# Kernel optimization log

Hardware: AMD Instinct MI355X
Metric: run time of the kernel (lower is better)

The kernel has to match this reference:

```python
import jax, jax.numpy as jnp
import numpy as np

MARGIN = 0.3
CLST_SCALE = 0.8
SEP_SCALE = 0.08
DIV_SCALE = 0.01
CONTRASTIVE_SCALE = 0.1


def setup_inputs() -> dict:
    key = jax.random.key(0)
    k1, k2, k3 = jax.random.split(key, 3)
    B, C, P, D = 16384, 100, 10, 256
    similarities = jax.random.uniform(k1, (B, C, P), jnp.float32, -1.0, 1.0)
    labels = jax.random.randint(k2, (B,), 0, C)
    prototypes = jax.random.normal(k3, (C * P, D), jnp.float32)
    starts = jnp.arange(C) * P
    proto_indices = jnp.stack([starts, starts + P], axis=1)  # [C,2] contiguous segments
    valid_mask = jnp.ones((C * P,), dtype=bool)
    return dict(similarities=similarities, labels=labels, prototypes=prototypes,
                proto_indices=proto_indices, valid_mask=valid_mask, max_prototypes=P)


def _balanced_proto_loss(similarities, prototypes, labels, proto_indices, valid_mask):
    B, C, P = similarities.shape
    T = prototypes.shape[0]
    distances = 1.0 - similarities  # [B,C,P]
    starts = proto_indices[:, 0]
    ends = proto_indices[:, 1]
    counts = ends - starts  # protos per class [C]
    INF = jnp.asarray(jnp.inf, distances.dtype)

    # mask invalid prototype slots per class, min over prototype slots
    pvalid = jnp.arange(P)[None, :] < counts[:, None]          # [C,P]
    dmask = jnp.where(pvalid[None, :, :], distances, INF)      # [B,C,P]
    min_all = jnp.min(dmask, axis=-1)                          # [B,C]

    # ---- cluster loss: min distance to own-class prototypes, class-balanced ----
    own_min = jnp.take_along_axis(min_all, labels[:, None], axis=1)[:, 0]  # [B]
    cls_n = jax.ops.segment_sum(jnp.ones_like(own_min), labels, num_segments=C)  # [C]
    cls_sum = jax.ops.segment_sum(own_min, labels, num_segments=C)
    has = cls_n > 0
    nvalid = jnp.maximum(jnp.sum(has), 1)
    mean_c = cls_sum / jnp.maximum(cls_n, 1.0)
    w = 1.0 / jnp.sqrt(cls_n + 1e-6)
    cluster_loss = jnp.sum(jnp.where(has, w * mean_c, 0.0)) / nvalid * CLST_SCALE

    # ---- separation loss: nearest prototype among all OTHER classes ----
    own_cls = jax.nn.one_hot(labels, C, dtype=bool)            # [B,C]
    other_min = jnp.min(jnp.where(own_cls, INF, min_all), axis=-1)  # [B]
    sep_term = jax.nn.relu(MARGIN - other_min)
    sep_cls_sum = jax.ops.segment_sum(sep_term, labels, num_segments=C)
    sep_loss = jnp.sum(jnp.where(has, sep_cls_sum / jnp.maximum(cls_n, 1.0), 0.0)) / nvalid * SEP_SCALE

    # ---- diversity loss: within-class prototype pairwise similarity (off-diagonal) ----
    norm = jnp.sqrt(jnp.sum(prototypes * prototypes, axis=-1, keepdims=True))
    pn = prototypes / jnp.maximum(norm, 1e-12)                 # F.normalize, eps=1e-12
    sim = pn @ pn.T                                            # [T,T]
    proto_class = jnp.searchsorted(starts, jnp.arange(T), side='right') - 1  # [T]
    same = proto_class[:, None] == proto_class[None, :]
    offdiag = ~jnp.eye(T, dtype=bool)
    pair = same & offdiag
    rel = jax.nn.relu(sim - 0.5)
    row_sum = jnp.sum(jnp.where(pair, rel, 0.0), axis=1)       # [T]
    cls_pair_sum = jax.ops.segment_sum(row_sum, proto_class, num_segments=C)
    npairs = (counts * (counts - 1)).astype(sim.dtype)
    div_valid = counts > 1
    ndv = jnp.maximum(jnp.sum(div_valid), 1)
    div_loss = jnp.sum(jnp.where(div_valid, cls_pair_sum / jnp.maximum(npairs, 1.0), 0.0)) / ndv * DIV_SCALE

    # ---- contrastive loss: mean off-diagonal sim over valid prototypes ----
    vpair = (valid_mask[:, None] & valid_mask[None, :]) & offdiag
    n_vpair = jnp.maximum(jnp.sum(vpair), 1).astype(sim.dtype)
    contrastive_loss = jnp.sum(jnp.where(vpair, sim, 0.0)) / n_vpair * CONTRASTIVE_SCALE

    total = cluster_loss + sep_loss + div_loss + contrastive_loss
    return jnp.stack([cluster_loss, sep_loss, div_loss, contrastive_loss, total])


def reference(similarities, labels, prototypes, proto_indices, valid_mask, max_prototypes):
    return _balanced_proto_loss(similarities, prototypes, labels, proto_indices, valid_mask)
```

## Files before the change

### kernel.cpp

```cpp
#include <hip/hip_runtime.h>
#include <hip/hip_bf16.h>
#include <math.h>

#define MARGIN_C 0.3f
#define CLST_SCALE 0.8f
#define SEP_SCALE 0.08f
#define DIV_SCALE 0.01f
#define CONTRASTIVE_SCALE 0.1f

#define INFF __builtin_huge_valf()
#define NVEC 16

__global__ __launch_bounds__(256) void norm_init_kernel(
    const float* __restrict__ protos, float* __restrict__ inv_norm,
    float* __restrict__ svec, double* __restrict__ diag,
    unsigned* __restrict__ done, int T, int D) {
    int t = threadIdx.x;
    if (blockIdx.x == 0) {
        for (int i = t; i < D; i += 256) svec[i] = 0.0f;
        if (t == 0) { *diag = 0.0; *done = 0u; }
    }
    int w = (blockIdx.x * 256 + t) >> 6;
    int lane = t & 63;
    if (w >= T) return;
    const float* row = protos + (size_t)w * D;
    float ss = 0.0f;
    if ((D & 3) == 0) {
        for (int k = lane * 4; k < D; k += 256) {
            float4 v = *reinterpret_cast<const float4*>(row + k);
            ss += v.x * v.x + v.y * v.y + v.z * v.z + v.w * v.w;
        }
    } else {
        for (int k = lane; k < D; k += 64) { float v = row[k]; ss += v * v; }
    }
#pragma unroll
    for (int off = 32; off > 0; off >>= 1) ss += __shfl_xor(ss, off);
    if (lane == 0) inv_norm[w] = 1.0f / fmaxf(sqrtf(ss), 1e-12f);
}

__global__ __launch_bounds__(256) void sample_kernel(
    const float* __restrict__ sims, const int* __restrict__ labels,
    const int* __restrict__ pidx,
    float* __restrict__ own_arr, float* __restrict__ sep_arr,
    int B, int C, int P) {
    int gid = blockIdx.x * 256 + threadIdx.x;
    int w = gid >> 6;
    int lane = threadIdx.x & 63;
    if (w >= B) return;
    int label = labels[w];
    const float* base = sims + (size_t)w * C * P;
    float own = INFF, other = INFF;
    for (int cc = 0; cc < C; cc += 64) {
        int c = cc + lane;
        if (c < C) {
            int cnt = pidx[2 * c + 1] - pidx[2 * c];
            const float* cb = base + (size_t)c * P;
            float m = INFF;
            if ((P & 1) == 0) {
                for (int p = 0; p < P; p += 2) {
                    float2 v = *reinterpret_cast<const float2*>(cb + p);
                    float d0 = (p < cnt) ? (1.0f - v.x) : INFF;
                    float d1 = (p + 1 < cnt) ? (1.0f - v.y) : INFF;
                    m = fminf(m, fminf(d0, d1));
                }
            } else {
                for (int p = 0; p < P; ++p) {
                    float v = cb[p];
                    m = fminf(m, (p < cnt) ? (1.0f - v) : INFF);
                }
            }
            if (c == label) own = m;
            else other = fminf(other, m);
        }
    }
#pragma unroll
    for (int off = 32; off > 0; off >>= 1) {
        own = fminf(own, __shfl_xor(own, off));
        other = fminf(other, __shfl_xor(other, off));
    }
    if (lane == 0) {
        own_arr[w] = own;
        sep_arr[w] = fmaxf(MARGIN_C - other, 0.0f);
    }
}

extern __shared__ float dynlds[];
__global__ __launch_bounds__(256) void mega_kernel(
    const int* __restrict__ labels, const float* __restrict__ own_arr,
    const float* __restrict__ sep_arr, const int* __restrict__ pidx,
    const int* __restrict__ vmask, const float* __restrict__ protos,
    const float* __restrict__ inv_norm,
    float* __restrict__ cls_sum, float* __restrict__ cls_n,
    float* __restrict__ sep_sum, float* __restrict__ cls_pair,
    float* __restrict__ svec, double* __restrict__ diag,
    unsigned* __restrict__ done, float* __restrict__ out,
    int B, int C, int T, int D, int P) {
    int t = threadIdx.x;
    int bid = blockIdx.x;
    int nb = 2 * C + NVEC;

    if (bid < C) {
        int c = bid;
        float o = 0.0f, sp = 0.0f, cn = 0.0f;
        for (int i = t; i < B; i += 256) {
            if (labels[i] == c) {
                o += own_arr[i];
                sp += sep_arr[i];
                cn += 1.0f;
            }
        }
#pragma unroll
        for (int off = 32; off > 0; off >>= 1) {
            o += __shfl_xor(o, off);
            sp += __shfl_xor(sp, off);
            cn += __shfl_xor(cn, off);
        }
        __shared__ float rs[3][4];
        if ((t & 63) == 0) { int wv = t >> 6; rs[0][wv] = o; rs[1][wv] = sp; rs[2][wv] = cn; }
        __syncthreads();
        if (t == 0) {
            cls_sum[c] = rs[0][0] + rs[0][1] + rs[0][2] + rs[0][3];
            sep_sum[c] = rs[1][0] + rs[1][1] + rs[1][2] + rs[1][3];
            cls_n[c] = rs[2][0] + rs[2][1] + rs[2][2] + rs[2][3];
        }
    } else if (bid < 2 * C) {
        int c = bid - C;
        int s0 = pidx[2 * c], e = pidx[2 * c + 1];
        int n = e - s0;
        if (n > P) n = P;
        if (n < 0) n = 0;
        int stride = D + 1;
        for (int idx = t; idx < n * D; idx += 256) {
            int i = (unsigned)idx / (unsigned)D;
            int d = idx - i * D;
            dynlds[i * stride + d] = protos[(size_t)(s0 + i) * D + d] * inv_norm[s0 + i];
        }
        __syncthreads();
        if (t < 64) {
            float tot = 0.0f;
            int npair = n * (n - 1) / 2;
            for (int l = t; l < npair; l += 64) {
                int i = 0, rem = l;
                while (rem >= n - 1 - i) { rem -= n - 1 - i; ++i; }
                int j = i + 1 + rem;
                float acc = 0.0f;
                for (int d = 0; d < D; ++d)
                    acc += dynlds[i * stride + d] * dynlds[j * stride + d];
                tot += 2.0f * fmaxf(acc - 0.5f, 0.0f);
            }
#pragma unroll
            for (int off = 32; off > 0; off >>= 1) tot += __shfl_xor(tot, off);
            if (t == 0) cls_pair[c] = tot;
        }
        __syncthreads();
    } else {
        int vb = bid - 2 * C;
        double ssq = 0.0;
        for (int d = t; d < D; d += 256) {
            float sv = 0.0f, sq = 0.0f;
            for (int r = vb; r < T; r += NVEC) {
                if (vmask[r] != 0) {
                    float v = protos[(size_t)r * D + d] * inv_norm[r];
                    sv += v;
                    sq += v * v;
                }
            }
            unsafeAtomicAdd(&svec[d], sv);
            ssq += (double)sq;
        }
#pragma unroll
        for (int off = 32; off > 0; off >>= 1) ssq += __shfl_xor(ssq, off);
        __shared__ double rd[4];
        if ((t & 63) == 0) rd[t >> 6] = ssq;
        __syncthreads();
        if (t == 0) unsafeAtomicAdd(diag, rd[0] + rd[1] + rd[2] + rd[3]);
    }

    __threadfence();
    __shared__ unsigned lastf;
    if (t == 0) lastf = (atomicAdd(done, 1u) == (unsigned)nb - 1u) ? 1u : 0u;
    __syncthreads();
    if (!lastf || t >= 64) return;
    __threadfence();
    int lane = t;
    float cl = 0.0f, sp = 0.0f, dv = 0.0f;
    int nval = 0, ndv = 0, V = 0;
    for (int c = lane; c < C; c += 64) {
        float n = cls_n[c];
        if (n > 0.0f) {
            nval += 1;
            float nm = fmaxf(n, 1.0f);
            float w = 1.0f / sqrtf(n + 1e-6f);
            cl += w * (cls_sum[c] / nm);
            sp += sep_sum[c] / nm;
        }
        int cnt = pidx[2 * c + 1] - pidx[2 * c];
        if (cnt > 1) {
            ndv += 1;
            float np = (float)(cnt * (cnt - 1));
            dv += cls_pair[c] / fmaxf(np, 1.0f);
        }
    }
    for (int r = lane; r < T; r += 64) V += (vmask[r] != 0) ? 1 : 0;
    double ss2 = 0.0;
    for (int d = lane; d < D; d += 64) { double v = (double)svec[d]; ss2 += v * v; }
#pragma unroll
    for (int off = 32; off > 0; off >>= 1) {
        cl += __shfl_xor(cl, off);
        sp += __shfl_xor(sp, off);
        dv += __shfl_xor(dv, off);
        nval += __shfl_xor(nval, off);
        ndv += __shfl_xor(ndv, off);
        V += __shfl_xor(V, off);
        ss2 += __shfl_xor(ss2, off);
    }
    if (lane == 0) {
        int nv = nval > 1 ? nval : 1;
        int nd = ndv > 1 ? ndv : 1;
        float cluster = cl / (float)nv * CLST_SCALE;
        float sep = sp / (float)nv * SEP_SCALE;
        float div = dv / (float)nd * DIV_SCALE;
        double contra_sum = ss2 - *diag;
        long long nvp = (long long)V * (long long)V - (long long)V;
        if (nvp < 1) nvp = 1;
        float contrastive = (float)(contra_sum / (double)nvp) * CONTRASTIVE_SCALE;
        out[0] = cluster;
        out[1] = sep;
        out[2] = div;
        out[3] = contrastive;
        out[4] = cluster + sep + div + contrastive;
    }
}

extern "C" void kernel_launch(void* const* d_in, const int* in_sizes, int n_in,
                              void* d_out, int out_size, void* d_ws, size_t ws_size,
                              hipStream_t stream) {
    const float* sims = (const float*)d_in[0];
    const int* labels = (const int*)d_in[1];
    const float* protos = (const float*)d_in[2];
    const int* pidx = (const int*)d_in[3];
    const int* vmask = (const int*)d_in[4];
    float* out = (float*)d_out;

    int B = in_sizes[1];
    int C = in_sizes[3] / 2;
    int T = in_sizes[4];
    int D = in_sizes[2] / T;
    int P = in_sizes[0] / (B * C);

    char* ws = (char*)d_ws;
    double* diag = (double*)ws;
    unsigned* done = (unsigned*)(ws + 8);
    float* cls_sum = (float*)(ws + 16);
    float* cls_n = cls_sum + C;
    float* sep_sum = cls_n + C;
    float* cls_pair = sep_sum + C;
    float* svec = cls_pair + C;
    float* inv_norm = svec + D;
    float* own_arr = inv_norm + T;
    float* sep_arr = own_arr + B;

    int nblk1 = (int)(((long long)T * 64 + 255) / 256);
    norm_init_kernel<<<dim3(nblk1), dim3(256), 0, stream>>>(
        protos, inv_norm, svec, diag, done, T, D);

    int nblk2 = (int)(((long long)B * 64 + 255) / 256);
    sample_kernel<<<dim3(nblk2), dim3(256), 0, stream>>>(
        sims, labels, pidx, own_arr, sep_arr, B, C, P);

    int nb3 = 2 * C + NVEC;
    size_t shm3 = (size_t)P * (size_t)(D + 1) * sizeof(float);
    mega_kernel<<<dim3(nb3), dim3(256), shm3, stream>>>(
        labels, own_arr, sep_arr, pidx, vmask, protos, inv_norm,
        cls_sum, cls_n, sep_sum, cls_pair, svec, diag, done, out,
        B, C, T, D, P);
}
```

Baseline: 152.2 us.

## Fuse norm and sample kernels, parallelize class reductions with LDS atomics

Merges the prototype-norm kernel and the per-sample min kernel into one launch, removing a kernel launch and its serialization. In the reduction kernel, the per-class scans (each of C blocks reading all B labels) become a segmented pass in which each block bins 256 samples into shared-memory class accumulators, then adds them to global memory with atomics. The diversity pair dot products now use all four wavefronts with float4 LDS reads and a cross-lane reduction, and the contrastive column sums use 64 blocks over contiguous row ranges. This adds global float atomics, so summation order is no longer deterministic.

Result: faster. 129.5 us (-14.9%).

```diff
diff --git a/kernel.cpp b/kernel.cpp
--- a/kernel.cpp
+++ b/kernel.cpp
@@ -9,43 +9,45 @@
 #define CONTRASTIVE_SCALE 0.1f
 
 #define INFF __builtin_huge_valf()
-#define NVEC 16
-
-__global__ __launch_bounds__(256) void norm_init_kernel(
-    const float* __restrict__ protos, float* __restrict__ inv_norm,
+#define NVEC 64
+
+__global__ __launch_bounds__(256) void front_kernel(
+    const float* __restrict__ sims, const int* __restrict__ labels,
+    const int* __restrict__ pidx, const float* __restrict__ protos,
+    float* __restrict__ inv_norm, float* __restrict__ own_arr,
+    float* __restrict__ sep_arr, float* __restrict__ cls3,
     float* __restrict__ svec, double* __restrict__ diag,
-    unsigned* __restrict__ done, int T, int D) {
+    unsigned* __restrict__ done, int B, int C, int T, int D, int P,
+    int nb_norm) {
     int t = threadIdx.x;
-    if (blockIdx.x == 0) {
-        for (int i = t; i < D; i += 256) svec[i] = 0.0f;
-        if (t == 0) { *diag = 0.0; *done = 0u; }
-    }
-    int w = (blockIdx.x * 256 + t) >> 6;
+    int bid = blockIdx.x;
+    if (bid < nb_norm) {
+        if (bid == 0) {
+            for (int i = t; i < 3 * C; i += 256) cls3[i] = 0.0f;
+            for (int i = t; i < D; i += 256) svec[i] = 0.0f;
+            if (t == 0) { *diag = 0.0; *done = 0u; }
+        }
+        int w = (bid * 256 + t) >> 6;
+        int lane = t & 63;
+        if (w >= T) return;
+        const float* row = protos + (size_t)w * D;
+        float ss = 0.0f;
+        if ((D & 3) == 0) {
+            for (int k = lane * 4; k < D; k += 256) {
+                float4 v = *reinterpret_cast<const float4*>(row + k);
+                ss += v.x * v.x + v.y * v.y + v.z * v.z + v.w * v.w;
+            }
+        } else {
+            for (int k = lane; k < D; k += 64) { float v = row[k]; ss += v * v; }
+        }
+#pragma unroll
+        for (int off = 32; off > 0; off >>= 1) ss += __shfl_xor(ss, off);
+        if (lane == 0) inv_norm[w] = 1.0f / fmaxf(sqrtf(ss), 1e-12f);
+        return;
+    }
+    int gid = (bid - nb_norm) * 256 + t;
+    int w = gid >> 6;
     int lane = t & 63;
-    if (w >= T) return;
-    const float* row = protos + (size_t)w * D;
-    float ss = 0.0f;
-    if ((D & 3) == 0) {
-        for (int k = lane * 4; k < D; k += 256) {
-            float4 v = *reinterpret_cast<const float4*>(row + k);
-            ss += v.x * v.x + v.y * v.y + v.z * v.z + v.w * v.w;
-        }
-    } else {
-        for (int k = lane; k < D; k += 64) { float v = row[k]; ss += v * v; }
-    }
-#pragma unroll
-    for (int off = 32; off > 0; off >>= 1) ss += __shfl_xor(ss, off);
-    if (lane == 0) inv_norm[w] = 1.0f / fmaxf(sqrtf(ss), 1e-12f);
-}
-
-__global__ __launch_bounds__(256) void sample_kernel(
-    const float* __restrict__ sims, const int* __restrict__ labels,
-    const int* __restrict__ pidx,
-    float* __restrict__ own_arr, float* __restrict__ sep_arr,
-    int B, int C, int P) {
-    int gid = blockIdx.x * 256 + threadIdx.x;
-    int w = gid >> 6;
-    int lane = threadIdx.x & 63;
     if (w >= B) return;
     int label = labels[w];
     const float* base = sims + (size_t)w * C * P;
@@ -84,107 +86,108 @@
     }
 }
 
-extern __shared__ float dynlds[];
-__global__ __launch_bounds__(256) void mega_kernel(
+__global__ __launch_bounds__(256) void reduce_kernel(
     const int* __restrict__ labels, const float* __restrict__ own_arr,
     const float* __restrict__ sep_arr, const int* __restrict__ pidx,
     const int* __restrict__ vmask, const float* __restrict__ protos,
     const float* __restrict__ inv_norm,
-    float* __restrict__ cls_sum, float* __restrict__ cls_n,
-    float* __restrict__ sep_sum, float* __restrict__ cls_pair,
+    float* __restrict__ cls3, float* __restrict__ cls_pair,
     float* __restrict__ svec, double* __restrict__ diag,
     unsigned* __restrict__ done, float* __restrict__ out,
-    int B, int C, int T, int D, int P) {
+    int B, int C, int T, int D, int P, int nSeg, unsigned nbTot) {
+    extern __shared__ float lds[];
+    __shared__ float wsum[4];
+    __shared__ double rd[4];
+    __shared__ unsigned lastf;
     int t = threadIdx.x;
     int bid = blockIdx.x;
-    int nb = 2 * C + NVEC;
-
-    if (bid < C) {
-        int c = bid;
-        float o = 0.0f, sp = 0.0f, cn = 0.0f;
-        for (int i = t; i < B; i += 256) {
-            if (labels[i] == c) {
-                o += own_arr[i];
-                sp += sep_arr[i];
-                cn += 1.0f;
-            }
-        }
-#pragma unroll
-        for (int off = 32; off > 0; off >>= 1) {
-            o += __shfl_xor(o, off);
-            sp += __shfl_xor(sp, off);
-            cn += __shfl_xor(cn, off);
-        }
-        __shared__ float rs[3][4];
-        if ((t & 63) == 0) { int wv = t >> 6; rs[0][wv] = o; rs[1][wv] = sp; rs[2][wv] = cn; }
-        __syncthreads();
-        if (t == 0) {
-            cls_sum[c] = rs[0][0] + rs[0][1] + rs[0][2] + rs[0][3];
-            sep_sum[c] = rs[1][0] + rs[1][1] + rs[1][2] + rs[1][3];
-            cls_n[c] = rs[2][0] + rs[2][1] + rs[2][2] + rs[2][3];
-        }
-    } else if (bid < 2 * C) {
-        int c = bid - C;
+
+    if (bid < nSeg) {
+        for (int i = t; i < 3 * C; i += 256) lds[i] = 0.0f;
+        __syncthreads();
+        int i = bid * 256 + t;
+        if (i < B) {
+            int lb = labels[i];
+            atomicAdd(&lds[lb], own_arr[i]);
+            atomicAdd(&lds[C + lb], 1.0f);
+            atomicAdd(&lds[2 * C + lb], sep_arr[i]);
+        }
+        __syncthreads();
+        for (int i2 = t; i2 < 3 * C; i2 += 256) {
+            float v = lds[i2];
+            if (v != 0.0f) unsafeAtomicAdd(&cls3[i2], v);
+        }
+    } else if (bid < nSeg + C) {
+        int c = bid - nSeg;
         int s0 = pidx[2 * c], e = pidx[2 * c + 1];
         int n = e - s0;
         if (n > P) n = P;
         if (n < 0) n = 0;
-        int stride = D + 1;
         for (int idx = t; idx < n * D; idx += 256) {
-            int i = (unsigned)idx / (unsigned)D;
-            int d = idx - i * D;
-            dynlds[i * stride + d] = protos[(size_t)(s0 + i) * D + d] * inv_norm[s0 + i];
-        }
-        __syncthreads();
-        if (t < 64) {
-            float tot = 0.0f;
-            int npair = n * (n - 1) / 2;
-            for (int l = t; l < npair; l += 64) {
-                int i = 0, rem = l;
-                while (rem >= n - 1 - i) { rem -= n - 1 - i; ++i; }
-                int j = i + 1 + rem;
-                float acc = 0.0f;
-                for (int d = 0; d < D; ++d)
-                    acc += dynlds[i * stride + d] * dynlds[j * stride + d];
-                tot += 2.0f * fmaxf(acc - 0.5f, 0.0f);
-            }
-#pragma unroll
-            for (int off = 32; off > 0; off >>= 1) tot += __shfl_xor(tot, off);
-            if (t == 0) cls_pair[c] = tot;
-        }
-        __syncthreads();
+            int i = (int)((unsigned)idx / (unsigned)D);
+            lds[idx] = protos[(size_t)s0 * D + idx] * inv_norm[s0 + i];
+        }
+        __syncthreads();
+        int wv = t >> 6, lane = t & 63;
+        int npair = n * (n - 1) / 2;
+        float tot = 0.0f;
+        for (int l = wv; l < npair; l += 4) {
+            int i = 0, rem = l;
+            while (rem >= n - 1 - i) { rem -= n - 1 - i; ++i; }
+            int j = i + 1 + rem;
+            float acc = 0.0f;
+            for (int q = lane * 4; q < D; q += 256) {
+                float4 a = *reinterpret_cast<const float4*>(&lds[i * D + q]);
+                float4 b = *reinterpret_cast<const float4*>(&lds[j * D + q]);
+                acc += a.x * b.x + a.y * b.y + a.z * b.z + a.w * b.w;
+            }
+#pragma unroll
+            for (int off = 32; off > 0; off >>= 1) acc += __shfl_xor(acc, off);
+            tot += 2.0f * fmaxf(acc - 0.5f, 0.0f);
+        }
+        if (lane == 0) wsum[wv] = tot;
+        __syncthreads();
+        if (t == 0) cls_pair[c] = wsum[0] + wsum[1] + wsum[2] + wsum[3];
     } else {
-        int vb = bid - 2 * C;
-        double ssq = 0.0;
+        int vb = bid - nSeg - C;
+        int rpb = (T + NVEC - 1) / NVEC;
+        int r0 = vb * rpb;
+        int r1 = r0 + rpb;
+        if (r1 > T) r1 = T;
+        double sqd = 0.0;
         for (int d = t; d < D; d += 256) {
             float sv = 0.0f, sq = 0.0f;
-            for (int r = vb; r < T; r += NVEC) {
+            for (int r = r0; r < r1; ++r) {
                 if (vmask[r] != 0) {
                     float v = protos[(size_t)r * D + d] * inv_norm[r];
                     sv += v;
                     sq += v * v;
                 }
             }
-            unsafeAtomicAdd(&svec[d], sv);
-            ssq += (double)sq;
-        }
-#pragma unroll
-        for (int off = 32; off > 0; off >>= 1) ssq += __shfl_xor(ssq, off);
-        __shared__ double rd[4];
-        if ((t & 63) == 0) rd[t >> 6] = ssq;
-        __syncthreads();
-        if (t == 0) unsafeAtomicAdd(diag, rd[0] + rd[1] + rd[2] + rd[3]);
+            if (sv != 0.0f) unsafeAtomicAdd(&svec[d], sv);
+            sqd += (double)sq;
+        }
+#pragma unroll
+        for (int off = 32; off > 0; off >>= 1) sqd += __shfl_xor(sqd, off);
+        if ((t & 63) == 0) rd[t >> 6] = sqd;
+        __syncthreads();
+        if (t == 0) {
+            double s = rd[0] + rd[1] + rd[2] + rd[3];
+            if (s != 0.0) unsafeAtomicAdd(diag, s);
+        }
     }
 
     __threadfence();
-    __shared__ unsigned lastf;
-    if (t == 0) lastf = (atomicAdd(done, 1u) == (unsigned)nb - 1u) ? 1u : 0u;
+    if (t == 0) lastf = (atomicAdd(done, 1u) == nbTot - 1u) ? 1u : 0u;
     __syncthreads();
     if (!lastf || t >= 64) return;
     __threadfence();
     int lane = t;
     float cl = 0.0f, sp = 0.0f, dv = 0.0f;
     int nval = 0, ndv = 0, V = 0;
+    const float* cls_sum = cls3;
+    const float* cls_n = cls3 + C;
+    const float* sep_sum = cls3 + 2 * C;
     for (int c = lane; c < C; c += 64) {
         float n = cls_n[c];
         if (n > 0.0f) {
@@ -251,27 +254,25 @@
     char* ws = (char*)d_ws;
     double* diag = (double*)ws;
     unsigned* done = (unsigned*)(ws + 8);
-    float* cls_sum = (float*)(ws + 16);
-    float* cls_n = cls_sum + C;
-    float* sep_sum = cls_n + C;
-    float* cls_pair = sep_sum + C;
+    float* cls3 = (float*)(ws + 16);
+    float* cls_pair = cls3 + 3 * C;
     float* svec = cls_pair + C;
     float* inv_norm = svec + D;
     float* own_arr = inv_norm + T;
     float* sep_arr = own_arr + B;
 
-    int nblk1 = (int)(((long long)T * 64 + 255) / 256);
-    norm_init_kernel<<<dim3(nblk1), dim3(256), 0, stream>>>(
-        protos, inv_norm, svec, diag, done, T, D);
-
-    int nblk2 = (int)(((long long)B * 64 + 255) / 256);
-    sample_kernel<<<dim3(nblk2), dim3(256), 0, stream>>>(
-        sims, labels, pidx, own_arr, sep_arr, B, C, P);
-
-    int nb3 = 2 * C + NVEC;
-    size_t shm3 = (size_t)P * (size_t)(D + 1) * sizeof(float);
-    mega_kernel<<<dim3(nb3), dim3(256), shm3, stream>>>(
+    int nb_norm = (int)(((long long)T * 64 + 255) / 256);
+    int nb_samp = (int)(((long long)B * 64 + 255) / 256);
+    front_kernel<<<dim3(nb_norm + nb_samp), dim3(256), 0, stream>>>(
+        sims, labels, pidx, protos, inv_norm, own_arr, sep_arr,
+        cls3, svec, diag, done, B, C, T, D, P, nb_norm);
+
+    int nSeg = (B + 255) / 256;
+    unsigned nbTot = (unsigned)(nSeg + C + NVEC);
+    int ldsf = 3 * C;
+    if (P * D > ldsf) ldsf = P * D;
+    size_t shm = (size_t)ldsf * sizeof(float);
+    reduce_kernel<<<dim3(nbTot), dim3(256), shm, stream>>>(
         labels, own_arr, sep_arr, pidx, vmask, protos, inv_norm,
-        cls_sum, cls_n, sep_sum, cls_pair, svec, diag, done, out,
-        B, C, T, D, P);
+        cls3, cls_pair, svec, diag, done, out, B, C, T, D, P, nSeg, nbTot);
 }
```
